# Performance work log

Measured on AMD Instinct MI355X. Metric: run time of the kernel, lower is better.

Reference implementation:

```python
import jax, jax.numpy as jnp
import numpy as np

B, T = 512, 100
STATE, LATENT, HIDDEN, EMBED, ACT = 200, 30, 200, 1024, 6


def _lin(k, out_dim, in_dim):
    return jax.random.normal(k, (out_dim, in_dim), jnp.float32) / np.sqrt(in_dim)


def setup_inputs() -> dict:
    key = jax.random.key(0)
    ks = jax.random.split(key, 12)
    return {
        "e": jax.random.normal(ks[0], (B, T + 1, EMBED), jnp.float32),
        "u": jax.random.normal(ks[1], (B, T, ACT), jnp.float32),
        "lat_act_W": _lin(ks[2], STATE, LATENT + ACT),
        "lat_act_b": jnp.zeros((STATE,), jnp.float32),
        "gru_Wih": _lin(ks[3], 3 * STATE, STATE),
        "gru_Whh": _lin(ks[4], 3 * STATE, STATE),
        "gru_bih": jnp.zeros((3 * STATE,), jnp.float32),
        "gru_bhh": jnp.zeros((3 * STATE,), jnp.float32),
        "prior1_W": _lin(ks[5], HIDDEN, STATE),
        "prior1_b": jnp.zeros((HIDDEN,), jnp.float32),
        "prior_m_W": _lin(ks[6], LATENT, HIDDEN),
        "prior_m_b": jnp.zeros((LATENT,), jnp.float32),
        "prior_s_W": _lin(ks[7], LATENT, HIDDEN),
        "prior_s_b": jnp.zeros((LATENT,), jnp.float32),
        "post1_W": _lin(ks[8], HIDDEN, STATE + EMBED),
        "post1_b": jnp.zeros((HIDDEN,), jnp.float32),
        "post_m_W": _lin(ks[9], LATENT, HIDDEN),
        "post_m_b": jnp.zeros((LATENT,), jnp.float32),
        "post_s_W": _lin(ks[10], LATENT, HIDDEN),
        "post_s_b": jnp.zeros((LATENT,), jnp.float32),
    }


def _std(raw):
    # softplus(raw) + 0.1, clamped to [1e-6, 10.0]
    return jnp.clip(jax.nn.softplus(raw) + 0.1, 1e-6, 10.0)


def reference(e, u, lat_act_W, lat_act_b, gru_Wih, gru_Whh, gru_bih, gru_bhh,
              prior1_W, prior1_b, prior_m_W, prior_m_b, prior_s_W, prior_s_b,
              post1_W, post1_b, post_m_W, post_m_b, post_s_W, post_s_b):
    Bx = u.shape[0]
    h0 = jnp.zeros((Bx, STATE), u.dtype)
    s0 = jnp.zeros((Bx, LATENT), u.dtype)
    u_t = jnp.swapaxes(u, 0, 1)            # [T, B, A]
    e_t = jnp.swapaxes(e[:, 1:], 0, 1)     # [T, B, E]

    def step(carry, inp):
        h, s = carry
        a, et = inp
        # deterministic_state_fwd
        x = jax.nn.relu(jnp.concatenate([s, a], axis=1) @ lat_act_W.T + lat_act_b)
        gi = x @ gru_Wih.T + gru_bih
        gh = h @ gru_Whh.T + gru_bhh
        ir, iz, inn = jnp.split(gi, 3, axis=1)
        hr, hz, hn = jnp.split(gh, 3, axis=1)
        r = jax.nn.sigmoid(ir + hr)
        z = jax.nn.sigmoid(iz + hz)
        n = jnp.tanh(inn + r * hn)
        h_new = (1.0 - z) * n + z * h
        # prior
        zp = jax.nn.relu(h_new @ prior1_W.T + prior1_b)
        pm = zp @ prior_m_W.T + prior_m_b
        ps = _std(zp @ prior_s_W.T + prior_s_b)
        # posterior
        zq = jax.nn.relu(jnp.concatenate([h_new, et], axis=1) @ post1_W.T + post1_b)
        qm = zq @ post_m_W.T + post_m_b
        qs = _std(zq @ post_s_W.T + post_s_b)
        return (h_new, qm), (h_new, pm, ps, qm, qs)

    _, (states, pm, ps, qm, qs) = jax.lax.scan(step, (h0, s0), (u_t, e_t))
    return states, pm, ps, qm, qs
```

## Files before the change

### kernel.cpp

```cpp
#include <hip/hip_runtime.h>
#include <cstdint>

typedef unsigned int u32;
typedef unsigned short u16;
typedef short bf16x8 __attribute__((ext_vector_type(8)));
typedef float f32x4 __attribute__((ext_vector_type(4)));

#define Bq 512
#define Tq 100
#define NST 200
#define NLAT 30
#define NEMB 1024
#define NACT 6

#define T_LA   0
#define T_IH   26
#define T_HH   299
#define T_P1   572
#define T_PM   663
#define T_POST 677
#define T_PR1  1093
#define T_TOT  1184
#define NFRAG  (T_TOT * 64)

__device__ __forceinline__ u16 f2bf(float f){
  u32 x = __float_as_uint(f);
  return (u16)((x + 0x7FFFu + ((x >> 16) & 1u)) >> 16);
}
__device__ __forceinline__ float bf2f(u16 h){ return __uint_as_float(((u32)h) << 16); }

__device__ __forceinline__ float fexp2(float x){ float r; asm("v_exp_f32 %0, %1" : "=v"(r) : "v"(x)); return r; }
__device__ __forceinline__ float frcp (float x){ float r; asm("v_rcp_f32 %0, %1" : "=v"(r) : "v"(x)); return r; }
#define LOG2E 1.44269504f
__device__ __forceinline__ float fsigm(float x){ return frcp(1.0f + fexp2(-LOG2E * x)); }
__device__ __forceinline__ float ftanh(float x){ return 1.0f - 2.0f * frcp(1.0f + fexp2(2.0f * LOG2E * x)); }

__device__ __forceinline__ float stdf_(float x){
  float sp = fmaxf(x, 0.f) + log1pf(expf(-fabsf(x))) + 0.1f;
  return fminf(fmaxf(sp, 1e-6f), 10.0f);
}

#define BAR() do { \
  asm volatile("s_waitcnt lgkmcnt(0)" ::: "memory"); \
  __builtin_amdgcn_s_barrier(); \
  asm volatile("" ::: "memory"); \
} while (0)

#define LOAD7(dst, base, unit) do { \
  const u16* _p = (base) + ((((size_t)(unit))*7) << 9) + lane*8; \
  _Pragma("unroll") \
  for (int _k = 0; _k < 7; ++_k) dst[_k] = *(const bf16x8*)(_p + ((size_t)_k << 9)); \
} while (0)

#define CHAIN7(accv, Afr, buf) do { \
  _Pragma("unroll") \
  for (int _k = 0; _k < 7; ++_k) \
    accv = __builtin_amdgcn_mfma_f32_16x16x32_bf16(Afr[_k], buf[_k], accv, 0, 0, 0); \
} while (0)

__global__ __launch_bounds__(256) void prep2(
    const float* __restrict__ lat_act_W,
    const float* __restrict__ gru_Wih,
    const float* __restrict__ gru_Whh,
    const float* __restrict__ post1_W,
    const float* __restrict__ post_m_W,
    const float* __restrict__ prior1_W,
    u16* __restrict__ wbuf)
{
  int gid = blockIdx.x * 256 + threadIdx.x;
  if (gid >= NFRAG) return;
  int tile = gid >> 6, lane = gid & 63;
  int nl = lane & 15, qq = lane >> 4;
  const float* src = nullptr;
  long stride = 0; int row = 0, kbase = 0, kmax = 0, coff = 0; bool vn = false;
  if (tile < T_IH){
    int lt = tile, nt = lt >> 1, kt = lt & 1;
    row = nt*16 + nl; vn = row < 200; kbase = kt*32 + qq*8; kmax = 36;
    src = lat_act_W; stride = 36;
  } else if (tile < T_HH){
    int lt = tile - T_IH, nt = lt / 7, kt = lt - nt*7;
    int g = nt / 3, gate = nt - g*3, nn = g*16 + nl;
    vn = nn < 200; row = gate*200 + nn; kbase = kt*32 + qq*8; kmax = 200;
    src = gru_Wih; stride = 200;
  } else if (tile < T_P1){
    int lt = tile - T_HH, nt = lt / 7, kt = lt - nt*7;
    int g = nt / 3, gate = nt - g*3, nn = g*16 + nl;
    vn = nn < 200; row = gate*200 + nn; kbase = kt*32 + qq*8; kmax = 200;
    src = gru_Whh; stride = 200;
  } else if (tile < T_PM){
    int lt = tile - T_P1, nt = lt / 7, kt = lt - nt*7;
    row = nt*16 + nl; vn = row < 200; kbase = kt*32 + qq*8; kmax = 200;
    src = post1_W; stride = 1224;
  } else if (tile < T_POST){
    int lt = tile - T_PM, nt = lt / 7, kt = lt - nt*7;
    row = nt*16 + nl; vn = row < 30; kbase = kt*32 + qq*8; kmax = 200;
    src = post_m_W; stride = 200;
  } else if (tile < T_PR1){
    int lt = tile - T_POST, nt = lt >> 5, kt = lt & 31;
    row = nt*16 + nl; vn = row < 200; kbase = kt*32 + qq*8; kmax = 1024; coff = 200;
    src = post1_W; stride = 1224;
  } else {
    int lt = tile - T_PR1, nt = lt / 7, kt = lt - nt*7;
    row = nt*16 + nl; vn = row < 200; kbase = kt*32 + qq*8; kmax = 200;
    src = prior1_W; stride = 200;
  }
  __align__(16) u16 ov[8];
  #pragma unroll
  for (int j = 0; j < 8; ++j){
    int k = kbase + j;
    float v = (vn && k < kmax) ? src[(size_t)row*stride + coff + k] : 0.f;
    ov[j] = f2bf(v);
  }
  *(uint4*)(wbuf + (size_t)gid*8) = *(const uint4*)ov;
}

__global__ __launch_bounds__(256) void epost_kernel(
    const float* __restrict__ e,
    const float* __restrict__ post1_b,
    const u16* __restrict__ wbuf,
    u16* __restrict__ Epost)
{
  const int tid = threadIdx.x;
  const int wave = tid >> 6, lane = tid & 63, nl = lane & 15, q = lane >> 4;
  const int m0 = blockIdx.x * 64;
  const int tt = m0 >> 9;
  const int b0 = (m0 & 511) + wave*16;
  const u16* wPOST = wbuf + (size_t)T_POST * 512 + lane*8;

  f32x4 acc[13];
  #pragma unroll
  for (int i = 0; i < 13; ++i) acc[i] = (f32x4){0.f,0.f,0.f,0.f};

  const float* arow = e + ((size_t)(b0 + nl)*(Tq + 1) + (tt + 1))*NEMB + q*8;

  for (int kt = 0; kt < 32; ++kt){
    float4 f0 = *(const float4*)(arow + (size_t)kt*32);
    float4 f1 = *(const float4*)(arow + (size_t)kt*32 + 4);
    bf16x8 afr;
    afr[0]=(short)f2bf(f0.x); afr[1]=(short)f2bf(f0.y); afr[2]=(short)f2bf(f0.z); afr[3]=(short)f2bf(f0.w);
    afr[4]=(short)f2bf(f1.x); afr[5]=(short)f2bf(f1.y); afr[6]=(short)f2bf(f1.z); afr[7]=(short)f2bf(f1.w);
    #pragma unroll
    for (int nt = 0; nt < 13; ++nt){
      bf16x8 b = *(const bf16x8*)(wPOST + (((size_t)(nt*32 + kt)) << 9));
      acc[nt] = __builtin_amdgcn_mfma_f32_16x16x32_bf16(afr, b, acc[nt], 0, 0, 0);
    }
  }
  #pragma unroll
  for (int nt = 0; nt < 13; ++nt){
    int n = nt*16 + nl;
    if (n < 200){
      float bb = post1_b[n];
      #pragma unroll
      for (int r = 0; r < 4; ++r){
        int m = m0 + wave*16 + q*4 + r;
        Epost[(size_t)m*NST + n] = f2bf(acc[nt][r] + bb);
      }
    }
  }
}

__global__ __launch_bounds__(512, 2) void core_kernel(
    const float* __restrict__ u,
    const float* __restrict__ lat_act_b,
    const float* __restrict__ gru_bih,
    const float* __restrict__ gru_bhh,
    const float* __restrict__ post_m_b,
    const u16* __restrict__ wbuf,
    const u16* __restrict__ Epost,
    float* __restrict__ out_states,
    float* __restrict__ out_qm)
{
  __shared__ __align__(16) u16 xs[16][72];
  __shared__ __align__(16) u16 xb[16][232];
  __shared__ __align__(16) u16 hb[2][16][232];
  __shared__ __align__(16) u16 zqb[16][232];

  const int tid  = threadIdx.x;
  const int wave = tid >> 6;
  const int lane = tid & 63;
  const int nl   = lane & 15;
  const int q    = lane >> 4;
  const int row0 = blockIdx.x * 16;

  const u16* wLA = wbuf + (size_t)T_LA * 512;
  const u16* wIH = wbuf + (size_t)T_IH * 512;
  const u16* wHH = wbuf + (size_t)T_HH * 512;
  const u16* wP1 = wbuf + (size_t)T_P1 * 512;
  const u16* wPM = wbuf + (size_t)T_PM * 512;

  const bool two  = (wave < 5);
  const int  cmax = two ? 2 : 1;

  bf16x8 b0[7], b1[7], b2[7];
  LOAD7(b0, wIH, wave*3);
  LOAD7(b1, wHH, wave*3);

  for (int i = tid; i < 16*72;  i += 512) ((u16*)xs)[i] = 0;
  for (int i = tid; i < 16*232; i += 512){
    ((u16*)xb)[i] = 0; ((u16*)hb[0])[i] = 0; ((u16*)hb[1])[i] = 0; ((u16*)zqb)[i] = 0;
  }

  bf16x8 laf[2][2] = {};
  float latb_r[2] = {0.f, 0.f};
  float brz_r[2][2] = {};
  float bin_r[2] = {}, bhn_r[2] = {};
  #pragma unroll
  for (int c = 0; c < 2; ++c){
    if (c < cmax){
      const int nt = wave + 8*c;
      #pragma unroll
      for (int kt = 0; kt < 2; ++kt)
        laf[c][kt] = *(const bf16x8*)(wLA + (((size_t)(nt*2 + kt)) << 9) + lane*8);
      const int n = nt*16 + nl;
      const bool v = (n < 200);
      latb_r[c] = v ? lat_act_b[n] : 0.f;
      if (v){
        brz_r[c][0] = gru_bih[n]       + gru_bhh[n];
        brz_r[c][1] = gru_bih[200 + n] + gru_bhh[200 + n];
        bin_r[c]    = gru_bih[400 + n];
        bhn_r[c]    = gru_bhh[400 + n];
      }
    }
  }
  float pmb_r = 0.f;
  { const int n2 = wave*16 + nl; if (wave < 2 && n2 < 30) pmb_r = post_m_b[n2]; }

  float hreg[2][4] = {};

  const int ur = tid / 6, uk = tid - ur*6;
  const bool uth = (tid < 96);
  float u_reg = uth ? u[((size_t)(row0 + ur)*Tq + 0)*NACT + uk] : 0.f;

  BAR();

  for (int t = 0; t < Tq; ++t){
    const int pb = t & 1;
    if (uth) xs[ur][30 + uk] = f2bf(u_reg);
    BAR();

    u32 ep0[4], ep1[4];
    {
      const int n0 = wave*16 + nl;
      const int n1 = n0 + 128;
      const u16* eb = Epost + ((size_t)t*Bq + row0 + q*4)*NST;
      #pragma unroll
      for (int r = 0; r < 4; ++r){
        ep0[r] = eb[(size_t)r*NST + n0];
        ep1[r] = (two && n1 < 200) ? (u32)eb[(size_t)r*NST + n1] : 0u;
      }
    }

    bf16x8 ah[7];
    #pragma unroll
    for (int kt = 0; kt < 7; ++kt)
      ah[kt] = *(const bf16x8*)(&hb[pb][nl][kt*32 + q*8]);

    {
      bf16x8 a0 = *(const bf16x8*)(&xs[nl][q*8]);
      bf16x8 a1 = *(const bf16x8*)(&xs[nl][32 + q*8]);
      #pragma unroll
      for (int c = 0; c < 2; ++c){
        if (c < cmax){
          f32x4 a = {0.f, 0.f, 0.f, 0.f};
          a = __builtin_amdgcn_mfma_f32_16x16x32_bf16(a0, laf[c][0], a, 0, 0, 0);
          a = __builtin_amdgcn_mfma_f32_16x16x32_bf16(a1, laf[c][1], a, 0, 0, 0);
          const int n = (wave + 8*c)*16 + nl;
          if (n < 200){
            #pragma unroll
            for (int r = 0; r < 4; ++r)
              xb[q*4 + r][n] = f2bf(fmaxf(a[r] + latb_r[c], 0.f));
          }
        }
      }
    }
    BAR();

    {
      bf16x8 ax[7];
      #pragma unroll
      for (int kt = 0; kt < 7; ++kt)
        ax[kt] = *(const bf16x8*)(&xb[nl][kt*32 + q*8]);
      if (uth && t + 1 < Tq) u_reg = u[((size_t)(row0 + ur)*Tq + (t + 1))*NACT + uk];

      float* os = out_states + ((size_t)t*Bq + row0)*NST;

      #pragma unroll
      for (int c = 0; c < 2; ++c){
        if (c < cmax){
          const int g  = wave + 8*c;
          const int gu = g*3;
          f32x4 acc0  = {0.f,0.f,0.f,0.f};
          f32x4 acc1  = {0.f,0.f,0.f,0.f};
          f32x4 acc2i = {0.f,0.f,0.f,0.f};
          f32x4 acc2h = {0.f,0.f,0.f,0.f};
          LOAD7(b2, wIH, gu + 1);  CHAIN7(acc0, ax, b0);
          LOAD7(b0, wHH, gu + 1);  CHAIN7(acc0, ah, b1);
          LOAD7(b1, wIH, gu + 2);  CHAIN7(acc1, ax, b2);
          LOAD7(b2, wHH, gu + 2);  CHAIN7(acc1, ah, b0);
          if (c == 0 && two) { LOAD7(b0, wIH, (wave + 8)*3); }
          else               { LOAD7(b0, wP1, wave); }
          CHAIN7(acc2i, ax, b1);
          if (c == 0 && two)      { LOAD7(b1, wHH, (wave + 8)*3); }
          else if (two)           { LOAD7(b1, wP1, wave + 8); }
          CHAIN7(acc2h, ah, b2);

          const int n = g*16 + nl;
          if (n < 200){
            #pragma unroll
            for (int r = 0; r < 4; ++r){
              const int m = q*4 + r;
              float rg = fsigm(acc0[r] + brz_r[c][0]);
              float zg = fsigm(acc1[r] + brz_r[c][1]);
              float ng = ftanh(acc2i[r] + bin_r[c] + rg*(acc2h[r] + bhn_r[c]));
              float hn = (1.f - zg)*ng + zg*hreg[c][r];
              hreg[c][r] = hn;
              hb[pb ^ 1][m][n] = f2bf(hn);
              os[(size_t)m*NST + n] = hn;
            }
          }
        }
      }
    }
    BAR();

    {
      bf16x8 ah2[7];
      #pragma unroll
      for (int kt = 0; kt < 7; ++kt)
        ah2[kt] = *(const bf16x8*)(&hb[pb ^ 1][nl][kt*32 + q*8]);
      f32x4 aP0 = {0.f,0.f,0.f,0.f}, aP1 = {0.f,0.f,0.f,0.f};
      if (wave < 2) { LOAD7(b2, wPM, wave); }
      CHAIN7(aP0, ah2, b0);
      LOAD7(b0, wIH, wave*3);
      if (two) { CHAIN7(aP1, ah2, b1); }
      LOAD7(b1, wHH, wave*3);
      {
        const int n0 = wave*16 + nl;
        #pragma unroll
        for (int r = 0; r < 4; ++r)
          zqb[q*4 + r][n0] = f2bf(fmaxf(aP0[r] + bf2f((u16)ep0[r]), 0.f));
        if (two){
          const int n1 = n0 + 128;
          if (n1 < 200){
            #pragma unroll
            for (int r = 0; r < 4; ++r)
              zqb[q*4 + r][n1] = f2bf(fmaxf(aP1[r] + bf2f((u16)ep1[r]), 0.f));
          }
        }
      }
    }
    BAR();

    if (wave < 2){
      bf16x8 az[7];
      #pragma unroll
      for (int kt = 0; kt < 7; ++kt)
        az[kt] = *(const bf16x8*)(&zqb[nl][kt*32 + q*8]);
      f32x4 aQ = {0.f,0.f,0.f,0.f};
      CHAIN7(aQ, az, b2);
      const int n = wave*16 + nl;
      if (n < 30){
        float* oq = out_qm + ((size_t)t*Bq + row0)*NLAT;
        #pragma unroll
        for (int r = 0; r < 4; ++r){
          const int m = q*4 + r;
          float v = aQ[r] + pmb_r;
          oq[(size_t)m*NLAT + n] = v;
          xs[m][n] = f2bf(v);
        }
      }
    }
  }
}

__global__ __launch_bounds__(256) void phasec_kernel(
    const float* __restrict__ states,
    const u16* __restrict__ Epost,
    const u16* __restrict__ wbuf,
    const float* __restrict__ prior1_b,
    const float* __restrict__ prior_m_W, const float* __restrict__ prior_m_b,
    const float* __restrict__ prior_s_W, const float* __restrict__ prior_s_b,
    const float* __restrict__ post_s_W,  const float* __restrict__ post_s_b,
    float* __restrict__ pm, float* __restrict__ ps, float* __restrict__ qs)
{
  __shared__ __align__(16) u16 stb[32][232];
  __shared__ float zp[32][208];
  __shared__ float zqf[32][208];
  __shared__ float hw[90][200];
  const int tid = threadIdx.x, wave = tid >> 6, lane = tid & 63, nl = lane & 15, q = lane >> 4;
  const size_t m0 = (size_t)blockIdx.x * 32;
  const u16* wP1  = wbuf + (size_t)T_P1 * 512;
  const u16* wPR1 = wbuf + (size_t)T_PR1 * 512;

  for (int i = tid; i < 32*200; i += 256){
    int r = i / 200, c = i - r*200;
    stb[r][c] = f2bf(states[(m0 + r)*NST + c]);
  }
  for (int i = tid; i < 32*32; i += 256){
    int r = i >> 5, c = i & 31;
    stb[r][200 + c] = 0;
  }
  for (int i = tid; i < 90*200; i += 256){
    int hl = i / 200, c = i - hl*200;
    const float* src = (hl < 30) ? prior_m_W : (hl < 60) ? prior_s_W : post_s_W;
    int l = (hl < 30) ? hl : (hl < 60) ? hl - 30 : hl - 60;
    ((float*)hw)[i] = src[(size_t)l*NST + c];
  }
  __syncthreads();

  {
    const int rowb = (wave & 1) * 16;
    const bool doZQ = (wave >= 2);
    const u16* wmat = doZQ ? wP1 : wPR1;
    bf16x8 a7[7];
    #pragma unroll
    for (int kt = 0; kt < 7; ++kt)
      a7[kt] = *(const bf16x8*)(&stb[rowb + nl][kt*32 + q*8]);
    for (int nt = 0; nt < 13; ++nt){
      f32x4 a = {0.f, 0.f, 0.f, 0.f};
      #pragma unroll
      for (int kt = 0; kt < 7; ++kt){
        bf16x8 b = *(const bf16x8*)(wmat + (((size_t)(nt*7 + kt)) << 9) + lane*8);
        a = __builtin_amdgcn_mfma_f32_16x16x32_bf16(a7[kt], b, a, 0, 0, 0);
      }
      int n = nt*16 + nl;
      if (n < 200){
        #pragma unroll
        for (int r = 0; r < 4; ++r){
          int m = rowb + q*4 + r;
          if (doZQ){
            float v = a[r] + bf2f(Epost[(m0 + m)*NST + n]);
            zqf[m][n] = fmaxf(v, 0.f);
          } else {
            float v = a[r] + prior1_b[n];
            zp[m][n] = fmaxf(v, 0.f);
          }
        }
      }
    }
  }
  __syncthreads();

  for (int i = tid; i < 32*90; i += 256){
    int r = i / 90, rem = i - r*90;
    int head = rem / 30, l = rem - head*30;
    const float* wrow = &hw[head*30 + l][0];
    const float* vec = (head == 2) ? &zqf[r][0] : &zp[r][0];
    float acc = 0.f;
    #pragma unroll 10
    for (int c = 0; c < 50; ++c){
      acc = fmaf(wrow[c*4 + 0], vec[c*4 + 0], acc);
      acc = fmaf(wrow[c*4 + 1], vec[c*4 + 1], acc);
      acc = fmaf(wrow[c*4 + 2], vec[c*4 + 2], acc);
      acc = fmaf(wrow[c*4 + 3], vec[c*4 + 3], acc);
    }
    float bias = (head == 0 ? prior_m_b : head == 1 ? prior_s_b : post_s_b)[l];
    float v = acc + bias;
    if (head) v = stdf_(v);
    float* o = head == 0 ? pm : head == 1 ? ps : qs;
    o[(m0 + r)*NLAT + l] = v;
  }
}

extern "C" void kernel_launch(void* const* d_in, const int* in_sizes, int n_in,
                              void* d_out, int out_size, void* d_ws, size_t ws_size,
                              hipStream_t stream)
{
  const float* e         = (const float*)d_in[0];
  const float* u         = (const float*)d_in[1];
  const float* lat_act_W = (const float*)d_in[2];
  const float* lat_act_b = (const float*)d_in[3];
  const float* gru_Wih   = (const float*)d_in[4];
  const float* gru_Whh   = (const float*)d_in[5];
  const float* gru_bih   = (const float*)d_in[6];
  const float* gru_bhh   = (const float*)d_in[7];
  const float* prior1_W  = (const float*)d_in[8];
  const float* prior1_b  = (const float*)d_in[9];
  const float* prior_m_W = (const float*)d_in[10];
  const float* prior_m_b = (const float*)d_in[11];
  const float* prior_s_W = (const float*)d_in[12];
  const float* prior_s_b = (const float*)d_in[13];
  const float* post1_W   = (const float*)d_in[14];
  const float* post1_b   = (const float*)d_in[15];
  const float* post_m_W  = (const float*)d_in[16];
  const float* post_m_b  = (const float*)d_in[17];
  const float* post_s_W  = (const float*)d_in[18];
  const float* post_s_b  = (const float*)d_in[19];

  float* out    = (float*)d_out;
  float* states = out;
  float* pm     = out + 10240000;
  float* ps     = out + 11776000;
  float* qm     = out + 13312000;
  float* qs     = out + 14848000;

  u16* Epost = (u16*)d_ws;
  u16* wbuf  = (u16*)((char*)d_ws + 20480000);

  hipLaunchKernelGGL(prep2, dim3((NFRAG + 255) / 256), dim3(256), 0, stream,
                     lat_act_W, gru_Wih, gru_Whh, post1_W, post_m_W, prior1_W, wbuf);

  hipLaunchKernelGGL(epost_kernel, dim3(800), dim3(256), 0, stream,
                     e, post1_b, wbuf, Epost);

  hipLaunchKernelGGL(core_kernel, dim3(32), dim3(512), 0, stream,
                     u, lat_act_b, gru_bih, gru_bhh, post_m_b, wbuf, Epost, states, qm);

  hipLaunchKernelGGL(phasec_kernel, dim3(1600), dim3(256), 0, stream,
                     states, Epost, wbuf, prior1_b,
                     prior_m_W, prior_m_b, prior_s_W, prior_s_b,
                     post_s_W, post_s_b, pm, ps, qs);
}
```

Baseline: 1.949 ms.

## Fold post_m projection into latent-action weights to shorten the recurrent step

Precomputes a combined weight lat_act_W[:, :30] @ post_m_W, applied directly to the zq hidden activations, so the recurrent loop no longer computes qm and drops one barrier and a serial matvec from each timestep. qm is now computed in the parallel post-pass kernel along with pm, ps and qs. The GRU weight-load pipeline is reordered and sched_barriers are added to overlap loads with MFMA chains. The trade-offs are a longer K=256 chain for the latent-action matmul and different bf16 rounding, since the folded weights are quantized once rather than qm being rounded before the matmul.

```diff
diff --git a/kernel.cpp b/kernel.cpp
--- a/kernel.cpp
+++ b/kernel.cpp
@@ -20,7 +20,8 @@
 #define T_PM   663
 #define T_POST 677
 #define T_PR1  1093
-#define T_TOT  1184
+#define T_CLA  1184
+#define T_TOT  1288
 #define NFRAG  (T_TOT * 64)
 
 __device__ __forceinline__ u16 f2bf(float f){
@@ -46,15 +47,29 @@
   asm volatile("" ::: "memory"); \
 } while (0)
 
+#define SB() __builtin_amdgcn_sched_barrier(0)
+
 #define LOAD7(dst, base, unit) do { \
   const u16* _p = (base) + ((((size_t)(unit))*7) << 9) + lane*8; \
   _Pragma("unroll") \
   for (int _k = 0; _k < 7; ++_k) dst[_k] = *(const bf16x8*)(_p + ((size_t)_k << 9)); \
 } while (0)
 
+#define LOAD8(dst, base, unit) do { \
+  const u16* _p = (base) + ((((size_t)(unit))*8) << 9) + lane*8; \
+  _Pragma("unroll") \
+  for (int _k = 0; _k < 8; ++_k) dst[_k] = *(const bf16x8*)(_p + ((size_t)_k << 9)); \
+} while (0)
+
 #define CHAIN7(accv, Afr, buf) do { \
   _Pragma("unroll") \
   for (int _k = 0; _k < 7; ++_k) \
+    accv = __builtin_amdgcn_mfma_f32_16x16x32_bf16(Afr[_k], buf[_k], accv, 0, 0, 0); \
+} while (0)
+
+#define CHAIN8(accv, Afr, buf) do { \
+  _Pragma("unroll") \
+  for (int _k = 0; _k < 8; ++_k) \
     accv = __builtin_amdgcn_mfma_f32_16x16x32_bf16(Afr[_k], buf[_k], accv, 0, 0, 0); \
 } while (0)
 
@@ -71,6 +86,34 @@
   if (gid >= NFRAG) return;
   int tile = gid >> 6, lane = gid & 63;
   int nl = lane & 15, qq = lane >> 4;
+
+  if (tile >= T_CLA){
+    int lt = tile - T_CLA, nt = lt >> 3, kt = lt & 7;
+    int row = nt*16 + nl;
+    bool vn = row < 200;
+    float wla[30];
+    #pragma unroll
+    for (int j = 0; j < 30; ++j) wla[j] = vn ? lat_act_W[(size_t)row*36 + j] : 0.f;
+    __align__(16) u16 ov[8];
+    #pragma unroll
+    for (int j = 0; j < 8; ++j){
+      float v = 0.f;
+      if (kt < 7){
+        int k = kt*32 + qq*8 + j;
+        if (vn && k < 200){
+          #pragma unroll
+          for (int j2 = 0; j2 < 30; ++j2) v += wla[j2] * post_m_W[(size_t)j2*200 + k];
+        }
+      } else {
+        int kk = qq*8 + j;
+        if (vn && kk < 6) v = lat_act_W[(size_t)row*36 + 30 + kk];
+      }
+      ov[j] = f2bf(v);
+    }
+    *(uint4*)(wbuf + (size_t)gid*8) = *(const uint4*)ov;
+    return;
+  }
+
   const float* src = nullptr;
   long stride = 0; int row = 0, kbase = 0, kmax = 0, coff = 0; bool vn = false;
   if (tile < T_IH){
@@ -162,15 +205,15 @@
 __global__ __launch_bounds__(512, 2) void core_kernel(
     const float* __restrict__ u,
     const float* __restrict__ lat_act_b,
+    const float* __restrict__ lat_act_W,
+    const float* __restrict__ post_m_b,
     const float* __restrict__ gru_bih,
     const float* __restrict__ gru_bhh,
-    const float* __restrict__ post_m_b,
     const u16* __restrict__ wbuf,
     const u16* __restrict__ Epost,
-    float* __restrict__ out_states,
-    float* __restrict__ out_qm)
+    float* __restrict__ out_states)
 {
-  __shared__ __align__(16) u16 xs[16][72];
+  __shared__ __align__(16) u16 xs[16][40];
   __shared__ __align__(16) u16 xb[16][232];
   __shared__ __align__(16) u16 hb[2][16][232];
   __shared__ __align__(16) u16 zqb[16][232];
@@ -182,39 +225,37 @@
   const int q    = lane >> 4;
   const int row0 = blockIdx.x * 16;
 
-  const u16* wLA = wbuf + (size_t)T_LA * 512;
-  const u16* wIH = wbuf + (size_t)T_IH * 512;
-  const u16* wHH = wbuf + (size_t)T_HH * 512;
-  const u16* wP1 = wbuf + (size_t)T_P1 * 512;
-  const u16* wPM = wbuf + (size_t)T_PM * 512;
+  const u16* wIH  = wbuf + (size_t)T_IH  * 512;
+  const u16* wHH  = wbuf + (size_t)T_HH  * 512;
+  const u16* wP1  = wbuf + (size_t)T_P1  * 512;
+  const u16* wCLA = wbuf + (size_t)T_CLA * 512;
 
   const bool two  = (wave < 5);
   const int  cmax = two ? 2 : 1;
 
-  bf16x8 b0[7], b1[7], b2[7];
-  LOAD7(b0, wIH, wave*3);
-  LOAD7(b1, wHH, wave*3);
-
-  for (int i = tid; i < 16*72;  i += 512) ((u16*)xs)[i] = 0;
+  bf16x8 b0[8], b1[8], b2[8];
+  LOAD8(b0, wCLA, wave);
+
+  for (int i = tid; i < 16*40;  i += 512) ((u16*)xs)[i] = 0;
   for (int i = tid; i < 16*232; i += 512){
     ((u16*)xb)[i] = 0; ((u16*)hb[0])[i] = 0; ((u16*)hb[1])[i] = 0; ((u16*)zqb)[i] = 0;
   }
 
-  bf16x8 laf[2][2] = {};
-  float latb_r[2] = {0.f, 0.f};
+  float latb_r[2]  = {0.f, 0.f};
+  float latb2_r[2] = {0.f, 0.f};
   float brz_r[2][2] = {};
   float bin_r[2] = {}, bhn_r[2] = {};
   #pragma unroll
   for (int c = 0; c < 2; ++c){
     if (c < cmax){
-      const int nt = wave + 8*c;
-      #pragma unroll
-      for (int kt = 0; kt < 2; ++kt)
-        laf[c][kt] = *(const bf16x8*)(wLA + (((size_t)(nt*2 + kt)) << 9) + lane*8);
-      const int n = nt*16 + nl;
+      const int n = (wave + 8*c)*16 + nl;
       const bool v = (n < 200);
-      latb_r[c] = v ? lat_act_b[n] : 0.f;
       if (v){
+        latb_r[c] = lat_act_b[n];
+        float s2 = 0.f;
+        #pragma unroll
+        for (int j = 0; j < 30; ++j) s2 += lat_act_W[(size_t)n*36 + j] * post_m_b[j];
+        latb2_r[c] = latb_r[c] + s2;
         brz_r[c][0] = gru_bih[n]       + gru_bhh[n];
         brz_r[c][1] = gru_bih[200 + n] + gru_bhh[200 + n];
         bin_r[c]    = gru_bih[400 + n];
@@ -222,8 +263,6 @@
       }
     }
   }
-  float pmb_r = 0.f;
-  { const int n2 = wave*16 + nl; if (wave < 2 && n2 < 30) pmb_r = post_m_b[n2]; }
 
   float hreg[2][4] = {};
 
@@ -235,7 +274,7 @@
 
   for (int t = 0; t < Tq; ++t){
     const int pb = t & 1;
-    if (uth) xs[ur][30 + uk] = f2bf(u_reg);
+    if (uth) xs[ur][uk] = f2bf(u_reg);
     BAR();
 
     u32 ep0[4], ep1[4];
@@ -256,19 +295,31 @@
       ah[kt] = *(const bf16x8*)(&hb[pb][nl][kt*32 + q*8]);
 
     {
-      bf16x8 a0 = *(const bf16x8*)(&xs[nl][q*8]);
-      bf16x8 a1 = *(const bf16x8*)(&xs[nl][32 + q*8]);
+      bf16x8 aL[8];
+      #pragma unroll
+      for (int kt = 0; kt < 7; ++kt)
+        aL[kt] = *(const bf16x8*)(&zqb[nl][kt*32 + q*8]);
+      aL[7] = *(const bf16x8*)(&xs[nl][q*8]);
+
+      f32x4 L0 = {0.f,0.f,0.f,0.f}, L1 = {0.f,0.f,0.f,0.f};
+      if (two) { LOAD8(b1, wCLA, wave + 8); }
+      LOAD7(b2, wIH, wave*3);
+      SB();
+      CHAIN8(L0, aL, b0);
+      LOAD7(b0, wHH, wave*3);
+      SB();
+      if (two) { CHAIN8(L1, aL, b1); }
+
       #pragma unroll
       for (int c = 0; c < 2; ++c){
         if (c < cmax){
-          f32x4 a = {0.f, 0.f, 0.f, 0.f};
-          a = __builtin_amdgcn_mfma_f32_16x16x32_bf16(a0, laf[c][0], a, 0, 0, 0);
-          a = __builtin_amdgcn_mfma_f32_16x16x32_bf16(a1, laf[c][1], a, 0, 0, 0);
+          const f32x4& L = c ? L1 : L0;
           const int n = (wave + 8*c)*16 + nl;
+          const float lb = (t == 0) ? latb_r[c] : latb2_r[c];
           if (n < 200){
             #pragma unroll
             for (int r = 0; r < 4; ++r)
-              xb[q*4 + r][n] = f2bf(fmaxf(a[r] + latb_r[c], 0.f));
+              xb[q*4 + r][n] = f2bf(fmaxf(L[r] + lb, 0.f));
           }
         }
       }
@@ -289,29 +340,31 @@
         if (c < cmax){
           const int g  = wave + 8*c;
           const int gu = g*3;
-          f32x4 acc0  = {0.f,0.f,0.f,0.f};
-          f32x4 acc1  = {0.f,0.f,0.f,0.f};
-          f32x4 acc2i = {0.f,0.f,0.f,0.f};
-          f32x4 acc2h = {0.f,0.f,0.f,0.f};
-          LOAD7(b2, wIH, gu + 1);  CHAIN7(acc0, ax, b0);
-          LOAD7(b0, wHH, gu + 1);  CHAIN7(acc0, ah, b1);
-          LOAD7(b1, wIH, gu + 2);  CHAIN7(acc1, ax, b2);
-          LOAD7(b2, wHH, gu + 2);  CHAIN7(acc1, ah, b0);
-          if (c == 0 && two) { LOAD7(b0, wIH, (wave + 8)*3); }
-          else               { LOAD7(b0, wP1, wave); }
-          CHAIN7(acc2i, ax, b1);
-          if (c == 0 && two)      { LOAD7(b1, wHH, (wave + 8)*3); }
-          else if (two)           { LOAD7(b1, wP1, wave + 8); }
-          CHAIN7(acc2h, ah, b2);
+          const bool last = (c + 1 == cmax);
+          f32x4 a0  = {0.f,0.f,0.f,0.f};
+          f32x4 a1  = {0.f,0.f,0.f,0.f};
+          f32x4 a2i = {0.f,0.f,0.f,0.f};
+          f32x4 a2h = {0.f,0.f,0.f,0.f};
+
+          LOAD7(b1, wIH, gu + 1);  SB();  CHAIN7(a0, ax, b2);
+          LOAD7(b2, wHH, gu + 1);  SB();  CHAIN7(a0, ah, b0);
+          LOAD7(b0, wIH, gu + 2);  SB();  CHAIN7(a1, ax, b1);
+          LOAD7(b1, wHH, gu + 2);  SB();  CHAIN7(a1, ah, b2);
+          if (last) { LOAD7(b2, wP1, wave); }
+          else      { LOAD7(b2, wIH, (wave + 8)*3); }
+          SB();  CHAIN7(a2i, ax, b0);
+          if (last) { LOAD8(b0, wCLA, wave); }
+          else      { LOAD7(b0, wHH, (wave + 8)*3); }
+          SB();  CHAIN7(a2h, ah, b1);
 
           const int n = g*16 + nl;
           if (n < 200){
             #pragma unroll
             for (int r = 0; r < 4; ++r){
               const int m = q*4 + r;
-              float rg = fsigm(acc0[r] + brz_r[c][0]);
-              float zg = fsigm(acc1[r] + brz_r[c][1]);
-              float ng = ftanh(acc2i[r] + bin_r[c] + rg*(acc2h[r] + bhn_r[c]));
+              float rg = fsigm(a0[r] + brz_r[c][0]);
+              float zg = fsigm(a1[r] + brz_r[c][1]);
+              float ng = ftanh(a2i[r] + bin_r[c] + rg*(a2h[r] + bhn_r[c]));
               float hn = (1.f - zg)*ng + zg*hreg[c][r];
               hreg[c][r] = hn;
               hb[pb ^ 1][m][n] = f2bf(hn);
@@ -329,11 +382,11 @@
       for (int kt = 0; kt < 7; ++kt)
         ah2[kt] = *(const bf16x8*)(&hb[pb ^ 1][nl][kt*32 + q*8]);
       f32x4 aP0 = {0.f,0.f,0.f,0.f}, aP1 = {0.f,0.f,0.f,0.f};
-      if (wave < 2) { LOAD7(b2, wPM, wave); }
-      CHAIN7(aP0, ah2, b0);
-      LOAD7(b0, wIH, wave*3);
+      if (two) { LOAD7(b1, wP1, wave + 8); }
+      SB();
+      CHAIN7(aP0, ah2, b2);
+      SB();
       if (two) { CHAIN7(aP1, ah2, b1); }
-      LOAD7(b1, wHH, wave*3);
       {
         const int n0 = wave*16 + nl;
         #pragma unroll
@@ -349,27 +402,6 @@
         }
       }
     }
-    BAR();
-
-    if (wave < 2){
-      bf16x8 az[7];
-      #pragma unroll
-      for (int kt = 0; kt < 7; ++kt)
-        az[kt] = *(const bf16x8*)(&zqb[nl][kt*32 + q*8]);
-      f32x4 aQ = {0.f,0.f,0.f,0.f};
-      CHAIN7(aQ, az, b2);
-      const int n = wave*16 + nl;
-      if (n < 30){
-        float* oq = out_qm + ((size_t)t*Bq + row0)*NLAT;
-        #pragma unroll
-        for (int r = 0; r < 4; ++r){
-          const int m = q*4 + r;
-          float v = aQ[r] + pmb_r;
-          oq[(size_t)m*NLAT + n] = v;
-          xs[m][n] = f2bf(v);
-        }
-      }
-    }
   }
 }
 
@@ -380,13 +412,14 @@
     const float* __restrict__ prior1_b,
     const float* __restrict__ prior_m_W, const float* __restrict__ prior_m_b,
     const float* __restrict__ prior_s_W, const float* __restrict__ prior_s_b,
+    const float* __restrict__ post_m_W,  const float* __restrict__ post_m_b,
     const float* __restrict__ post_s_W,  const float* __restrict__ post_s_b,
-    float* __restrict__ pm, float* __restrict__ ps, float* __restrict__ qs)
+    float* __restrict__ pm, float* __restrict__ ps,
+    float* __restrict__ qm, float* __restrict__ qs)
 {
   __shared__ __align__(16) u16 stb[32][232];
   __shared__ float zp[32][208];
   __shared__ float zqf[32][208];
-  __shared__ float hw[90][200];
   const int tid = threadIdx.x, wave = tid >> 6, lane = tid & 63, nl = lane & 15, q = lane >> 4;
   const size_t m0 = (size_t)blockIdx.x * 32;
   const u16* wP1  = wbuf + (size_t)T_P1 * 512;
@@ -399,12 +432,6 @@
   for (int i = tid; i < 32*32; i += 256){
     int r = i >> 5, c = i & 31;
     stb[r][200 + c] = 0;
-  }
-  for (int i = tid; i < 90*200; i += 256){
-    int hl = i / 200, c = i - hl*200;
-    const float* src = (hl < 30) ? prior_m_W : (hl < 60) ? prior_s_W : post_s_W;
-    int l = (hl < 30) ? hl : (hl < 60) ? hl - 30 : hl - 60;
-    ((float*)hw)[i] = src[(size_t)l*NST + c];
   }
   __syncthreads();
 
@@ -441,23 +468,26 @@
   }
   __syncthreads();
 
-  for (int i = tid; i < 32*90; i += 256){
-    int r = i / 90, rem = i - r*90;
+  for (int i = tid; i < 32*120; i += 256){
+    int r = i / 120, rem = i - r*120;
     int head = rem / 30, l = rem - head*30;
-    const float* wrow = &hw[head*30 + l][0];
-    const float* vec = (head == 2) ? &zqf[r][0] : &zp[r][0];
+    const float* wrow = (head == 0 ? prior_m_W : head == 1 ? prior_s_W :
+                         head == 2 ? post_m_W  : post_s_W) + (size_t)l*NST;
+    const float* vec = (head >= 2) ? &zqf[r][0] : &zp[r][0];
     float acc = 0.f;
     #pragma unroll 10
     for (int c = 0; c < 50; ++c){
-      acc = fmaf(wrow[c*4 + 0], vec[c*4 + 0], acc);
-      acc = fmaf(wrow[c*4 + 1], vec[c*4 + 1], acc);
-      acc = fmaf(wrow[c*4 + 2], vec[c*4 + 2], acc);
-      acc = fmaf(wrow[c*4 + 3], vec[c*4 + 3], acc);
-    }
-    float bias = (head == 0 ? prior_m_b : head == 1 ? prior_s_b : post_s_b)[l];
+      float4 wv = *(const float4*)(wrow + c*4);
+      acc = fmaf(wv.x, vec[c*4 + 0], acc);
+      acc = fmaf(wv.y, vec[c*4 + 1], acc);
+      acc = fmaf(wv.z, vec[c*4 + 2], acc);
+      acc = fmaf(wv.w, vec[c*4 + 3], acc);
+    }
+    float bias = (head == 0 ? prior_m_b : head == 1 ? prior_s_b :
+                  head == 2 ? post_m_b  : post_s_b)[l];
     float v = acc + bias;
-    if (head) v = stdf_(v);
-    float* o = head == 0 ? pm : head == 1 ? ps : qs;
+    if (head == 1 || head == 3) v = stdf_(v);
+    float* o = head == 0 ? pm : head == 1 ? ps : head == 2 ? qm : qs;
     o[(m0 + r)*NLAT + l] = v;
   }
 }
@@ -504,10 +534,12 @@
                      e, post1_b, wbuf, Epost);
 
   hipLaunchKernelGGL(core_kernel, dim3(32), dim3(512), 0, stream,
-                     u, lat_act_b, gru_bih, gru_bhh, post_m_b, wbuf, Epost, states, qm);
+                     u, lat_act_b, lat_act_W, post_m_b, gru_bih, gru_bhh,
+                     wbuf, Epost, states);
 
   hipLaunchKernelGGL(phasec_kernel, dim3(1600), dim3(256), 0, stream,
                      states, Epost, wbuf, prior1_b,
                      prior_m_W, prior_m_b, prior_s_W, prior_s_b,
-                     post_s_W, post_s_b, pm, ps, qs);
-}
+                     post_m_W, post_m_b, post_s_W, post_s_b,
+                     pm, ps, qm, qs);
+}
```

Result: slower. 2.151 ms (+10.4%).
